# Optimization experiments

Hardware: AMD Instinct MI355X
Metric: run time of the kernel (lower is better)

## Reference

```python
import jax, jax.numpy as jnp
import numpy as np

B, S, D = 1, 2048, 4096
N_Q, N_KV, HD = 32, 8, 128
N_REP = N_Q // N_KV
WINDOW = 1024
NEG = -1e9


def setup_inputs() -> dict:
    key = jax.random.key(0)
    ks = jax.random.split(key, 6)
    x = jax.random.normal(ks[0], (B, S, D), dtype=jnp.float32)
    # RoPE frequencies (Llama-style): theta = 10000^{-2i/HD}
    inv_freq = 1.0 / (10000.0 ** (np.arange(0, HD, 2, dtype=np.float32) / HD))
    t = np.arange(S, dtype=np.float32)
    ang = np.outer(t, inv_freq)  # [S, HD//2]
    freqs_cos = jnp.asarray(np.cos(ang), dtype=jnp.float32)
    freqs_sin = jnp.asarray(np.sin(ang), dtype=jnp.float32)
    # additive causal mask [S, S]: 0 on/below diag, -1e9 above
    mask = jnp.where(jnp.tril(jnp.ones((S, S), dtype=bool)), 0.0, NEG).astype(jnp.float32)
    scale = 0.02
    w_q = jax.random.normal(ks[1], (D, N_Q * HD), dtype=jnp.float32) * scale
    w_k = jax.random.normal(ks[2], (D, N_KV * HD), dtype=jnp.float32) * scale
    w_v = jax.random.normal(ks[3], (D, N_KV * HD), dtype=jnp.float32) * scale
    w_o = jax.random.normal(ks[4], (N_Q * HD, D), dtype=jnp.float32) * scale
    return {"x": x, "freqs_cos": freqs_cos, "freqs_sin": freqs_sin, "mask": mask,
            "w_q": w_q, "w_k": w_k, "w_v": w_v, "w_o": w_o}


def _rope(t, cos, sin):
    # t: [B, S, H, HD]; cos/sin: [S, HD//2] -> complex multiply on pairs
    tp = t.reshape(*t.shape[:-1], HD // 2, 2)
    e, o = tp[..., 0], tp[..., 1]
    c = cos[None, :, None, :]
    s = sin[None, :, None, :]
    re = e * c - o * s
    ro = e * s + o * c
    return jnp.stack([re, ro], axis=-1).reshape(t.shape)


def reference(x, freqs_cos, freqs_sin, mask, w_q, w_k, w_v, w_o):
    b, s, _ = x.shape
    xq = (x @ w_q).reshape(b, s, N_Q, HD)
    xk = (x @ w_k).reshape(b, s, N_KV, HD)
    xv = (x @ w_v).reshape(b, s, N_KV, HD)
    xq = _rope(xq, freqs_cos, freqs_sin)
    xk = _rope(xk, freqs_cos, freqs_sin)
    # GQA head repeat
    keys = jnp.repeat(xk, N_REP, axis=2)    # [b, s, N_Q, HD]
    values = jnp.repeat(xv, N_REP, axis=2)
    q = xq.transpose(0, 2, 1, 3)            # [b, h, s, hd]
    k = keys.transpose(0, 2, 1, 3)
    v = values.transpose(0, 2, 1, 3)
    scores = jnp.einsum('bhqd,bhkd->bhqk', q, k) / jnp.sqrt(jnp.float32(HD))
    scores = scores + mask[None, None, :, :]
    # sliding-window band: attend only to keys within WINDOW positions back
    idx = jnp.arange(s)
    diff = idx[:, None] - idx[None, :]
    sliding = (diff >= 0) & (diff < WINDOW)
    scores = jnp.where(sliding[None, None, :, :], scores, NEG)
    probs = jax.nn.softmax(scores, axis=-1).astype(q.dtype)
    out = jnp.einsum('bhqk,bhkd->bhqd', probs, v)
    out = out.transpose(0, 2, 1, 3).reshape(b, s, N_Q * HD)
    return out @ w_o
```

## Files before the change

### kernel.cpp

```cpp
#include <hip/hip_runtime.h>

typedef unsigned short u16;
typedef unsigned int u32;
typedef __bf16 bf16x8 __attribute__((ext_vector_type(8)));
typedef __bf16 bf16x4 __attribute__((ext_vector_type(4)));
typedef float f32x4 __attribute__((ext_vector_type(4)));

#define MFMA16(a, b, c) __builtin_amdgcn_mfma_f32_16x16x32_bf16(a, b, c, 0, 0, 0)

__device__ __forceinline__ u16 f2bf(float f) {
  u32 u = __float_as_uint(f);
  u += 0x7FFFu + ((u >> 16) & 1u);
  return (u16)(u >> 16);
}
__device__ __forceinline__ float bf2f(u16 h) {
  return __uint_as_float(((u32)h) << 16);
}

__device__ __forceinline__ void gload_lds16(const u16* g, u16* l) {
  __builtin_amdgcn_global_load_lds((__attribute__((address_space(1))) void*)g,
                                   (__attribute__((address_space(3))) void*)l,
                                   16, 0, 0);
}

__global__ __launch_bounds__(256) void cvt_x(const float* __restrict__ in,
                                             u16* __restrict__ out) {
  int i = (blockIdx.x * 256 + threadIdx.x) * 4;
  float4 v = *(const float4*)&in[i];
  ushort4 o;
  o.x = f2bf(v.x);
  o.y = f2bf(v.y);
  o.z = f2bf(v.z);
  o.w = f2bf(v.w);
  *(ushort4*)&out[i] = o;
}

__global__ __launch_bounds__(256) void tbf_f2b(const float* __restrict__ in,
                                               u16* __restrict__ out,
                                               int ldin, int ldout) {
  __shared__ float tile[64][65];
  const int t = threadIdx.x;
  const int c4 = t & 15;
  const int rb = t >> 4;
  const int r0 = blockIdx.y * 64;
  const int c0 = blockIdx.x * 64;
#pragma unroll
  for (int p = 0; p < 4; p++) {
    int r = p * 16 + rb;
    float4 v = *(const float4*)&in[(size_t)(r0 + r) * ldin + c0 + c4 * 4];
    tile[r][c4 * 4 + 0] = v.x;
    tile[r][c4 * 4 + 1] = v.y;
    tile[r][c4 * 4 + 2] = v.z;
    tile[r][c4 * 4 + 3] = v.w;
  }
  __syncthreads();
#pragma unroll
  for (int p = 0; p < 4; p++) {
    int oc = p * 16 + rb;
    ushort4 v;
    v.x = f2bf(tile[c4 * 4 + 0][oc]);
    v.y = f2bf(tile[c4 * 4 + 1][oc]);
    v.z = f2bf(tile[c4 * 4 + 2][oc]);
    v.w = f2bf(tile[c4 * 4 + 3][oc]);
    *(ushort4*)&out[(size_t)(c0 + oc) * ldout + r0 + c4 * 4] = v;
  }
}

__global__ __launch_bounds__(256) void tbf_b(const u16* __restrict__ in,
                                             u16* __restrict__ out,
                                             int ldin, int ldout) {
  __shared__ u16 tile[64][68];
  const int t = threadIdx.x;
  const int c4 = t & 15;
  const int rb = t >> 4;
  const int r0 = blockIdx.y * 64;
  const int c0 = blockIdx.x * 64;
#pragma unroll
  for (int p = 0; p < 4; p++) {
    int r = p * 16 + rb;
    ushort4 v = *(const ushort4*)&in[(size_t)(r0 + r) * ldin + c0 + c4 * 4];
    *(ushort4*)&tile[r][c4 * 4] = v;
  }
  __syncthreads();
#pragma unroll
  for (int p = 0; p < 4; p++) {
    int oc = p * 16 + rb;
    ushort4 v;
    v.x = tile[c4 * 4 + 0][oc];
    v.y = tile[c4 * 4 + 1][oc];
    v.z = tile[c4 * 4 + 2][oc];
    v.w = tile[c4 * 4 + 3][oc];
    *(ushort4*)&out[(size_t)(c0 + oc) * ldout + r0 + c4 * 4] = v;
  }
}

template <int BN, int F32OUT>
__global__ __launch_bounds__(512, 2) void gemm256(const u16* __restrict__ A,
                                                  const u16* __restrict__ B,
                                                  void* __restrict__ Cv,
                                                  int K, int ldc) {
  constexpr int NJ = BN / 64;
  __shared__ __attribute__((aligned(16))) u16 As[2][256 * 64];
  __shared__ __attribute__((aligned(16))) u16 Bs[2][BN * 64];
  const int tid = threadIdx.x;
  const int wave = tid >> 6;
  const int lane = tid & 63;
  const int l16 = lane & 15;
  const int quad = lane >> 4;
  const int wm = wave >> 2;
  const int wn = wave & 3;
  const int id = blockIdx.y * gridDim.x + blockIdx.x;
  const int bm = (id & 7) * 256;
  const int bn0 = (id >> 3) * BN;

  const u16* srcA[4];
  const u16* srcB[NJ];
#pragma unroll
  for (int m = 0; m < 4; m++) {
    int c = (wave * 4 + m) * 64 + lane;
    int r = c >> 3;
    int hl = (c & 7) ^ (r & 7);
    srcA[m] = A + (size_t)(bm + r) * K + hl * 8;
  }
#pragma unroll
  for (int m = 0; m < NJ; m++) {
    int c = (wave * NJ + m) * 64 + lane;
    int r = c >> 3;
    int hl = (c & 7) ^ (r & 7);
    srcB[m] = B + (size_t)(bn0 + r) * K + hl * 8;
  }

  f32x4 acc[8][NJ];
#pragma unroll
  for (int i = 0; i < 8; i++)
#pragma unroll
    for (int j = 0; j < NJ; j++) acc[i][j] = (f32x4){0.f, 0.f, 0.f, 0.f};

  auto stage = [&](int nb) {
#pragma unroll
    for (int m = 0; m < 4; m++) {
      gload_lds16(srcA[m], &As[nb][(size_t)((wave * 4 + m) * 64 + lane) * 8]);
      srcA[m] += 64;
    }
#pragma unroll
    for (int m = 0; m < NJ; m++) {
      gload_lds16(srcB[m], &Bs[nb][(size_t)((wave * NJ + m) * 64 + lane) * 8]);
      srcB[m] += 64;
    }
  };

  stage(0);
  const int NT = K >> 6;
  int cur = 0;
  for (int t = 0; t < NT; ++t) {
    if (t + 1 < NT) {
      stage(cur ^ 1);
      if constexpr (NJ == 3)
        asm volatile("s_waitcnt vmcnt(7)" ::: "memory");
      else
        asm volatile("s_waitcnt vmcnt(6)" ::: "memory");
    } else {
      asm volatile("s_waitcnt vmcnt(0)" ::: "memory");
    }
    __builtin_amdgcn_s_barrier();
    __builtin_amdgcn_sched_barrier(0);
    const u16* as = &As[cur][0];
    const u16* bs = &Bs[cur][0];
#pragma unroll
    for (int ks = 0; ks < 2; ks++) {
      bf16x8 bfr[NJ];
#pragma unroll
      for (int j = 0; j < NJ; j++) {
        int r = wn * (BN / 4) + j * 16 + l16;
        int h = (ks * 4 + quad) ^ (r & 7);
        bfr[j] = *(const bf16x8*)&bs[r * 64 + h * 8];
      }
#pragma unroll
      for (int ih = 0; ih < 2; ih++) {
        bf16x8 afr[4];
#pragma unroll
        for (int i = 0; i < 4; i++) {
          int r = wm * 128 + ih * 64 + i * 16 + l16;
          int h = (ks * 4 + quad) ^ (r & 7);
          afr[i] = *(const bf16x8*)&as[r * 64 + h * 8];
        }
        __builtin_amdgcn_s_setprio(1);
#pragma unroll
        for (int i = 0; i < 4; i++)
#pragma unroll
          for (int j = 0; j < NJ; j++)
            acc[ih * 4 + i][j] = MFMA16(afr[i], bfr[j], acc[ih * 4 + i][j]);
        __builtin_amdgcn_s_setprio(0);
      }
    }
    __builtin_amdgcn_sched_barrier(0);
    __builtin_amdgcn_s_barrier();
    cur ^= 1;
  }

  const int wcol = bn0 + wn * (BN / 4);
  if constexpr (F32OUT) {
    float* C = (float*)Cv;
#pragma unroll
    for (int ih = 0; ih < 2; ih++)
#pragma unroll
      for (int i = 0; i < 4; i++)
#pragma unroll
        for (int j = 0; j < NJ; j++)
#pragma unroll
          for (int r = 0; r < 4; r++) {
            int row = bm + wm * 128 + ih * 64 + i * 16 + quad * 4 + r;
            int col = wcol + j * 16 + l16;
            C[(size_t)row * ldc + col] = acc[ih * 4 + i][j][r];
          }
  } else {
    u16* C = (u16*)Cv;
#pragma unroll
    for (int ih = 0; ih < 2; ih++)
#pragma unroll
      for (int i = 0; i < 4; i++)
#pragma unroll
        for (int j = 0; j < NJ; j++)
#pragma unroll
          for (int r = 0; r < 4; r++) {
            int row = bm + wm * 128 + ih * 64 + i * 16 + quad * 4 + r;
            int col = wcol + j * 16 + l16;
            C[(size_t)row * ldc + col] = f2bf(acc[ih * 4 + i][j][r]);
          }
  }
}

__global__ __launch_bounds__(256) void rope_k(u16* __restrict__ qkv,
                                              const float* __restrict__ fc,
                                              const float* __restrict__ fs) {
  int idx = blockIdx.x * 256 + threadIdx.x;
  int j = idx & 63;
  int rem = idx >> 6;
  int head = rem % 40;
  int s = rem / 40;
  float c = fc[s * 64 + j];
  float sn = fs[s * 64 + j];
  int col = (head < 32) ? (head * 128 + 2 * j) : (4096 + (head - 32) * 128 + 2 * j);
  u32* p = (u32*)&qkv[(size_t)s * 6144 + col];
  u32 v = *p;
  float e = bf2f((u16)(v & 0xFFFFu));
  float o = bf2f((u16)(v >> 16));
  float re = e * c - o * sn;
  float ro = e * sn + o * c;
  *p = (u32)f2bf(re) | ((u32)f2bf(ro) << 16);
}

__global__ __launch_bounds__(256) void attn_k(const u16* __restrict__ qkv,
                                              const u16* __restrict__ vt,
                                              u16* __restrict__ outb) {
  __shared__ __attribute__((aligned(16))) u16 Kb[2][32 * 128];
  __shared__ __attribute__((aligned(16))) u16 Vb[2][128 * 32];
  __shared__ __attribute__((aligned(16))) u16 plds[4][32 * 36];
  const int h = blockIdx.x;
  const int q0 = blockIdx.y * 128;
  const int t = threadIdx.x;
  const int wave = t >> 6;
  const int lane = t & 63;
  const int l16 = lane & 15;
  const int quad = lane >> 4;
  const int hkv = h >> 2;
  const int qw = q0 + wave * 32;
  u16* myp = &plds[wave][0];

  bf16x8 qa[2][4];
#pragma unroll
  for (int i = 0; i < 2; i++)
#pragma unroll
    for (int kc = 0; kc < 4; kc++)
      qa[i][kc] = *(const bf16x8*)&qkv[(size_t)(qw + i * 16 + l16) * 6144 +
                                       h * 128 + kc * 32 + quad * 8];

  f32x4 o[2][8];
#pragma unroll
  for (int i = 0; i < 2; i++)
#pragma unroll
    for (int d = 0; d < 8; d++) o[i][d] = (f32x4){0.f, 0.f, 0.f, 0.f};
  float lloc[2][4] = {{0.f, 0.f, 0.f, 0.f}, {0.f, 0.f, 0.f, 0.f}};

  const int kb_start = (q0 - 1023 > 0 ? q0 - 1023 : 0) & ~31;
  const int kb_last = q0 + 96;
  const float sc = 0.08838834764831845f;

  const int kr0 = t >> 4, kc0s = t & 15;
  const int kr1 = (256 + t) >> 4, kc1s = t & 15;
  const int vr0 = t >> 2, vc0s = t & 3;
  const int vr1 = (256 + t) >> 2, vc1s = t & 3;
  const u16* kg = qkv + 4096 + hkv * 128;
  const u16* vg = vt + (size_t)hkv * 128 * 2048;

#define STAGE(kb_, nb_)                                                        \
  do {                                                                         \
    int kb__ = (kb_);                                                          \
    gload_lds16(&kg[(size_t)(kb__ + kr0) * 6144 + (kc0s ^ (kr0 & 15)) * 8],    \
                &Kb[nb_][t * 8]);                                              \
    gload_lds16(&kg[(size_t)(kb__ + kr1) * 6144 + (kc1s ^ (kr1 & 15)) * 8],    \
                &Kb[nb_][2048 + t * 8]);                                       \
    gload_lds16(&vg[(size_t)vr0 * 2048 + kb__ + (vc0s ^ (vr0 & 3)) * 8],       \
                &Vb[nb_][t * 8]);                                              \
    gload_lds16(&vg[(size_t)vr1 * 2048 + kb__ + (vc1s ^ (vr1 & 3)) * 8],       \
                &Vb[nb_][2048 + t * 8]);                                       \
  } while (0)

  STAGE(kb_start, 0);
  int cur = 0;

  for (int kb = kb_start; kb <= kb_last; kb += 32) {
    __syncthreads();
    if (kb + 32 <= kb_last) STAGE(kb + 32, cur ^ 1);
    const u16* kcur = &Kb[cur][0];
    const u16* vcur = &Vb[cur][0];

    f32x4 s0[2] = {(f32x4){0.f, 0.f, 0.f, 0.f}, (f32x4){0.f, 0.f, 0.f, 0.f}};
    f32x4 s1[2] = {(f32x4){0.f, 0.f, 0.f, 0.f}, (f32x4){0.f, 0.f, 0.f, 0.f}};
#pragma unroll
    for (int kc = 0; kc < 4; kc++) {
      int ch = ((kc * 4 + quad) ^ l16) * 8;
      bf16x8 b0 = *(const bf16x8*)&kcur[l16 * 128 + ch];
      bf16x8 b1 = *(const bf16x8*)&kcur[(l16 + 16) * 128 + ch];
      s0[0] = MFMA16(qa[0][kc], b0, s0[0]);
      s1[0] = MFMA16(qa[0][kc], b1, s1[0]);
      s0[1] = MFMA16(qa[1][kc], b0, s0[1]);
      s1[1] = MFMA16(qa[1][kc], b1, s1[1]);
    }

    float p0[2][4], p1[2][4];
    bool fast = (kb + 31 <= qw) && (qw + 31 - kb <= 1023);
    if (fast) {
#pragma unroll
      for (int i = 0; i < 2; i++)
#pragma unroll
        for (int r = 0; r < 4; r++) {
          p0[i][r] = __expf(s0[i][r] * sc);
          p1[i][r] = __expf(s1[i][r] * sc);
        }
    } else {
#pragma unroll
      for (int i = 0; i < 2; i++)
#pragma unroll
        for (int r = 0; r < 4; r++) {
          int row = qw + i * 16 + quad * 4 + r;
          int col0 = kb + l16;
          int col1 = col0 + 16;
          bool v0 = (col0 <= row) && (row - col0 < 1024);
          bool v1 = (col1 <= row) && (row - col1 < 1024);
          p0[i][r] = v0 ? __expf(s0[i][r] * sc) : 0.f;
          p1[i][r] = v1 ? __expf(s1[i][r] * sc) : 0.f;
        }
    }
#pragma unroll
    for (int i = 0; i < 2; i++)
#pragma unroll
      for (int r = 0; r < 4; r++) {
        lloc[i][r] += p0[i][r] + p1[i][r];
        myp[(i * 16 + quad * 4 + r) * 36 + l16] = f2bf(p0[i][r]);
        myp[(i * 16 + quad * 4 + r) * 36 + l16 + 16] = f2bf(p1[i][r]);
      }
    asm volatile("s_waitcnt lgkmcnt(0)" ::: "memory");
    bf16x8 pa[2];
#pragma unroll
    for (int i = 0; i < 2; i++) {
      bf16x4 lo = *(const bf16x4*)&myp[(i * 16 + l16) * 36 + quad * 8];
      bf16x4 hi = *(const bf16x4*)&myp[(i * 16 + l16) * 36 + quad * 8 + 4];
#pragma unroll
      for (int j = 0; j < 4; j++) {
        pa[i][j] = lo[j];
        pa[i][j + 4] = hi[j];
      }
    }
#pragma unroll
    for (int d = 0; d < 8; d++) {
      int rv = l16 + 16 * d;
      bf16x8 vb = *(const bf16x8*)&vcur[rv * 32 + ((quad ^ (l16 & 3)) * 8)];
      o[0][d] = MFMA16(pa[0], vb, o[0][d]);
      o[1][d] = MFMA16(pa[1], vb, o[1][d]);
    }
    cur ^= 1;
  }

#pragma unroll
  for (int i = 0; i < 2; i++) {
    float inv[4];
#pragma unroll
    for (int r = 0; r < 4; r++) {
      float l = lloc[i][r];
#pragma unroll
      for (int m = 8; m >= 1; m >>= 1) l += __shfl_xor(l, m, 64);
      inv[r] = 1.0f / l;
    }
#pragma unroll
    for (int d = 0; d < 8; d++)
#pragma unroll
      for (int r = 0; r < 4; r++) {
        int row = qw + i * 16 + quad * 4 + r;
        outb[(size_t)row * 4096 + h * 128 + d * 16 + l16] =
            f2bf(o[i][d][r] * inv[r]);
      }
  }
#undef STAGE
}

extern "C" void kernel_launch(void* const* d_in, const int* in_sizes, int n_in,
                              void* d_out, int out_size, void* d_ws, size_t ws_size,
                              hipStream_t stream) {
  const float* x = (const float*)d_in[0];
  const float* fc = (const float*)d_in[1];
  const float* fs = (const float*)d_in[2];
  const float* wq = (const float*)d_in[4];
  const float* wk = (const float*)d_in[5];
  const float* wv = (const float*)d_in[6];
  const float* wo = (const float*)d_in[7];
  float* outp = (float*)d_out;
  char* ws = (char*)d_ws;
  u16* xb = (u16*)(ws);
  u16* wqkvT = (u16*)(ws + 16777216);
  u16* qkvb = (u16*)(ws + 67108864);
  u16* vtb = (u16*)(ws + 92274688);
  u16* aout = (u16*)(ws + 96468992);

  cvt_x<<<8192, 256, 0, stream>>>(x, xb);
  tbf_f2b<<<dim3(64, 64), 256, 0, stream>>>(wq, wqkvT, 4096, 4096);
  tbf_f2b<<<dim3(16, 64), 256, 0, stream>>>(wk, wqkvT + (size_t)4096 * 4096,
                                            1024, 4096);
  tbf_f2b<<<dim3(16, 64), 256, 0, stream>>>(wv, wqkvT + (size_t)5120 * 4096,
                                            1024, 4096);
  gemm256<192, 0><<<dim3(32, 8), 512, 0, stream>>>(xb, wqkvT, qkvb, 4096, 6144);
  rope_k<<<20480, 256, 0, stream>>>(qkvb, fc, fs);
  tbf_b<<<dim3(16, 32), 256, 0, stream>>>(qkvb + 5120, vtb, 6144, 2048);
  tbf_f2b<<<dim3(64, 64), 256, 0, stream>>>(wo, wqkvT, 4096, 4096);
  attn_k<<<dim3(32, 16), 256, 0, stream>>>(qkvb, vtb, aout);
  gemm256<128, 1><<<dim3(32, 8), 512, 0, stream>>>(aout, wqkvT, outp, 4096,
                                                   4096);
}
```

Measured before the change: 507.0 us.

## Rewrite GEMMs with triple-buffered K=32 pipeline, new warp layout and block swizzle

Replaces the double-buffered K=64 GEMM with a templated triple-buffered K=32 version that prefetches two stages ahead and drops the trailing barrier per iteration. It also changes the warp tiling (4x2 or 2x4 waves), uses a new XOR swizzle for the 32-wide LDS rows, and adds a grouped block-to-tile mapping for L2 locality. The output projection now uses 128x256 tiles instead of 256x128. The aim is to hide global load latency and cut barrier stalls. In exchange it adds more waitcnt bookkeeping, with per-wave counts for partial B loads, and shorter MFMA bursts per barrier.

```diff
diff --git a/kernel.cpp b/kernel.cpp
--- a/kernel.cpp
+++ b/kernel.cpp
@@ -94,139 +94,143 @@
   }
 }
 
-template <int BN, int F32OUT>
-__global__ __launch_bounds__(512, 2) void gemm256(const u16* __restrict__ A,
-                                                  const u16* __restrict__ B,
-                                                  void* __restrict__ Cv,
-                                                  int K, int ldc) {
-  constexpr int NJ = BN / 64;
-  __shared__ __attribute__((aligned(16))) u16 As[2][256 * 64];
-  __shared__ __attribute__((aligned(16))) u16 Bs[2][BN * 64];
+template <int BM, int BN, int WM, int WN, int F32OUT>
+__global__ __launch_bounds__(512, 2) void gemm3(const u16* __restrict__ A,
+                                                const u16* __restrict__ B,
+                                                void* __restrict__ Cv,
+                                                int K, int ldc) {
+  constexpr int R = BM / WM / 16;
+  constexpr int C = BN / WN / 16;
+  constexpr int LA = (BM * 4) / 512;
+  constexpr int EXTRA = BN * 4 - 512;
+  constexpr int MG = (2048 / BM) / 8;
+  __shared__ __attribute__((aligned(16))) u16 As[3][BM * 32];
+  __shared__ __attribute__((aligned(16))) u16 Bs[3][BN * 32];
   const int tid = threadIdx.x;
   const int wave = tid >> 6;
   const int lane = tid & 63;
   const int l16 = lane & 15;
   const int quad = lane >> 4;
-  const int wm = wave >> 2;
-  const int wn = wave & 3;
-  const int id = blockIdx.y * gridDim.x + blockIdx.x;
-  const int bm = (id & 7) * 256;
-  const int bn0 = (id >> 3) * BN;
-
-  const u16* srcA[4];
-  const u16* srcB[NJ];
-#pragma unroll
-  for (int m = 0; m < 4; m++) {
-    int c = (wave * 4 + m) * 64 + lane;
-    int r = c >> 3;
-    int hl = (c & 7) ^ (r & 7);
+  const int wm = wave / WN;
+  const int wn = wave % WN;
+  const int id = blockIdx.x;
+  const int bm = ((id & 7) * MG + ((id >> 3) % MG)) * BM;
+  const int bn0 = ((id >> 3) / MG) * BN;
+
+  const u16* srcA[LA];
+#pragma unroll
+  for (int m = 0; m < LA; m++) {
+    int c = m * 512 + tid;
+    int r = c >> 2;
+    int hl = (c & 3) ^ (r & 3) ^ ((r >> 2) & 3);
     srcA[m] = A + (size_t)(bm + r) * K + hl * 8;
   }
-#pragma unroll
-  for (int m = 0; m < NJ; m++) {
-    int c = (wave * NJ + m) * 64 + lane;
-    int r = c >> 3;
-    int hl = (c & 7) ^ (r & 7);
-    srcB[m] = B + (size_t)(bn0 + r) * K + hl * 8;
-  }
-
-  f32x4 acc[8][NJ];
-#pragma unroll
-  for (int i = 0; i < 8; i++)
-#pragma unroll
-    for (int j = 0; j < NJ; j++) acc[i][j] = (f32x4){0.f, 0.f, 0.f, 0.f};
-
-  auto stage = [&](int nb) {
-#pragma unroll
-    for (int m = 0; m < 4; m++) {
-      gload_lds16(srcA[m], &As[nb][(size_t)((wave * 4 + m) * 64 + lane) * 8]);
-      srcA[m] += 64;
-    }
-#pragma unroll
-    for (int m = 0; m < NJ; m++) {
-      gload_lds16(srcB[m], &Bs[nb][(size_t)((wave * NJ + m) * 64 + lane) * 8]);
-      srcB[m] += 64;
+  const u16* srcB0;
+  const u16* srcB1;
+  {
+    int c = tid, r = c >> 2;
+    int hl = (c & 3) ^ (r & 3) ^ ((r >> 2) & 3);
+    srcB0 = B + (size_t)(bn0 + r) * K + hl * 8;
+    c = 512 + tid;
+    r = c >> 2;
+    int r2 = r < BN ? r : 0;
+    hl = (c & 3) ^ (r2 & 3) ^ ((r2 >> 2) & 3);
+    srcB1 = B + (size_t)(bn0 + r2) * K + hl * 8;
+  }
+
+  f32x4 acc[R][C];
+#pragma unroll
+  for (int i = 0; i < R; i++)
+#pragma unroll
+    for (int j = 0; j < C; j++) acc[i][j] = (f32x4){0.f, 0.f, 0.f, 0.f};
+
+  auto stage = [&](int kt, int nb2) {
+    const int ko = kt * 32;
+#pragma unroll
+    for (int m = 0; m < LA; m++)
+      gload_lds16(srcA[m] + ko, &As[nb2][(m * 512 + tid) * 8]);
+    gload_lds16(srcB0 + ko, &Bs[nb2][tid * 8]);
+    if constexpr (EXTRA == 512) {
+      gload_lds16(srcB1 + ko, &Bs[nb2][(512 + tid) * 8]);
+    } else if constexpr (EXTRA > 0) {
+      if (tid < EXTRA) gload_lds16(srcB1 + ko, &Bs[nb2][(512 + tid) * 8]);
     }
   };
 
-  stage(0);
-  const int NT = K >> 6;
-  int cur = 0;
+  const int NT = K >> 5;
+  stage(0, 0);
+  stage(1, 1);
+  int nb = 0, ns = 2;
   for (int t = 0; t < NT; ++t) {
-    if (t + 1 < NT) {
-      stage(cur ^ 1);
-      if constexpr (NJ == 3)
-        asm volatile("s_waitcnt vmcnt(7)" ::: "memory");
+    if (t == NT - 1) {
+      asm volatile("s_waitcnt vmcnt(0)" ::: "memory");
+    } else if constexpr (EXTRA == 512) {
+      asm volatile("s_waitcnt vmcnt(3)" ::: "memory");
+    } else {
+      if (wave < 4)
+        asm volatile("s_waitcnt vmcnt(4)" ::: "memory");
       else
-        asm volatile("s_waitcnt vmcnt(6)" ::: "memory");
-    } else {
-      asm volatile("s_waitcnt vmcnt(0)" ::: "memory");
-    }
+        asm volatile("s_waitcnt vmcnt(3)" ::: "memory");
+    }
+    __builtin_amdgcn_sched_barrier(0);
     __builtin_amdgcn_s_barrier();
     __builtin_amdgcn_sched_barrier(0);
-    const u16* as = &As[cur][0];
-    const u16* bs = &Bs[cur][0];
-#pragma unroll
-    for (int ks = 0; ks < 2; ks++) {
-      bf16x8 bfr[NJ];
-#pragma unroll
-      for (int j = 0; j < NJ; j++) {
-        int r = wn * (BN / 4) + j * 16 + l16;
-        int h = (ks * 4 + quad) ^ (r & 7);
-        bfr[j] = *(const bf16x8*)&bs[r * 64 + h * 8];
-      }
-#pragma unroll
-      for (int ih = 0; ih < 2; ih++) {
-        bf16x8 afr[4];
-#pragma unroll
-        for (int i = 0; i < 4; i++) {
-          int r = wm * 128 + ih * 64 + i * 16 + l16;
-          int h = (ks * 4 + quad) ^ (r & 7);
-          afr[i] = *(const bf16x8*)&as[r * 64 + h * 8];
+    if (t + 2 < NT) stage(t + 2, ns);
+
+    const u16* as = &As[nb][0];
+    const u16* bs = &Bs[nb][0];
+    bf16x8 bfr[C];
+#pragma unroll
+    for (int j = 0; j < C; j++) {
+      int r = wn * (C * 16) + j * 16 + l16;
+      bfr[j] = *(const bf16x8*)&bs[r * 32 +
+                                   ((quad ^ (r & 3) ^ ((r >> 2) & 3)) << 3)];
+    }
+    bf16x8 afr[R];
+#pragma unroll
+    for (int i = 0; i < R; i++) {
+      int r = wm * (R * 16) + i * 16 + l16;
+      afr[i] = *(const bf16x8*)&as[r * 32 +
+                                   ((quad ^ (r & 3) ^ ((r >> 2) & 3)) << 3)];
+    }
+    __builtin_amdgcn_s_setprio(1);
+#pragma unroll
+    for (int i = 0; i < R; i++)
+#pragma unroll
+      for (int j = 0; j < C; j++)
+        acc[i][j] = MFMA16(afr[i], bfr[j], acc[i][j]);
+    __builtin_amdgcn_s_setprio(0);
+    __builtin_amdgcn_sched_barrier(0);
+    nb = (nb == 2) ? 0 : nb + 1;
+    ns = (ns == 2) ? 0 : ns + 1;
+  }
+
+  const int crow0 = bm + wm * (R * 16);
+  const int ccol0 = bn0 + wn * (C * 16);
+  if constexpr (F32OUT) {
+    float* Cp = (float*)Cv;
+#pragma unroll
+    for (int i = 0; i < R; i++)
+#pragma unroll
+      for (int j = 0; j < C; j++)
+#pragma unroll
+        for (int rr = 0; rr < 4; rr++) {
+          int row = crow0 + i * 16 + quad * 4 + rr;
+          int col = ccol0 + j * 16 + l16;
+          Cp[(size_t)row * ldc + col] = acc[i][j][rr];
         }
-        __builtin_amdgcn_s_setprio(1);
-#pragma unroll
-        for (int i = 0; i < 4; i++)
-#pragma unroll
-          for (int j = 0; j < NJ; j++)
-            acc[ih * 4 + i][j] = MFMA16(afr[i], bfr[j], acc[ih * 4 + i][j]);
-        __builtin_amdgcn_s_setprio(0);
-      }
-    }
-    __builtin_amdgcn_sched_barrier(0);
-    __builtin_amdgcn_s_barrier();
-    cur ^= 1;
-  }
-
-  const int wcol = bn0 + wn * (BN / 4);
-  if constexpr (F32OUT) {
-    float* C = (float*)Cv;
-#pragma unroll
-    for (int ih = 0; ih < 2; ih++)
-#pragma unroll
-      for (int i = 0; i < 4; i++)
-#pragma unroll
-        for (int j = 0; j < NJ; j++)
-#pragma unroll
-          for (int r = 0; r < 4; r++) {
-            int row = bm + wm * 128 + ih * 64 + i * 16 + quad * 4 + r;
-            int col = wcol + j * 16 + l16;
-            C[(size_t)row * ldc + col] = acc[ih * 4 + i][j][r];
-          }
   } else {
-    u16* C = (u16*)Cv;
-#pragma unroll
-    for (int ih = 0; ih < 2; ih++)
-#pragma unroll
-      for (int i = 0; i < 4; i++)
-#pragma unroll
-        for (int j = 0; j < NJ; j++)
-#pragma unroll
-          for (int r = 0; r < 4; r++) {
-            int row = bm + wm * 128 + ih * 64 + i * 16 + quad * 4 + r;
-            int col = wcol + j * 16 + l16;
-            C[(size_t)row * ldc + col] = f2bf(acc[ih * 4 + i][j][r]);
-          }
+    u16* Cp = (u16*)Cv;
+#pragma unroll
+    for (int i = 0; i < R; i++)
+#pragma unroll
+      for (int j = 0; j < C; j++)
+#pragma unroll
+        for (int rr = 0; rr < 4; rr++) {
+          int row = crow0 + i * 16 + quad * 4 + rr;
+          int col = ccol0 + j * 16 + l16;
+          Cp[(size_t)row * ldc + col] = f2bf(acc[i][j][rr]);
+        }
   }
 }
 
@@ -428,11 +432,12 @@
                                             1024, 4096);
   tbf_f2b<<<dim3(16, 64), 256, 0, stream>>>(wv, wqkvT + (size_t)5120 * 4096,
                                             1024, 4096);
-  gemm256<192, 0><<<dim3(32, 8), 512, 0, stream>>>(xb, wqkvT, qkvb, 4096, 6144);
+  gemm3<256, 192, 4, 2, 0><<<256, 512, 0, stream>>>(xb, wqkvT, qkvb, 4096,
+                                                    6144);
   rope_k<<<20480, 256, 0, stream>>>(qkvb, fc, fs);
   tbf_b<<<dim3(16, 32), 256, 0, stream>>>(qkvb + 5120, vtb, 6144, 2048);
   tbf_f2b<<<dim3(64, 64), 256, 0, stream>>>(wo, wqkvT, 4096, 4096);
   attn_k<<<dim3(32, 16), 256, 0, stream>>>(qkvb, vtb, aout);
-  gemm256<128, 1><<<dim3(32, 8), 512, 0, stream>>>(aout, wqkvT, outp, 4096,
-                                                   4096);
-}
+  gemm3<128, 256, 2, 4, 1><<<256, 512, 0, stream>>>(aout, wqkvT, outp, 4096,
+                                                    4096);
+}
```

After: 561.0 us. 10.6% more time.
